# Optimization experiments

Hardware: AMD Instinct MI355X
Metric: run time of the kernel (lower is better)

The kernel has to match this reference:

```python
import jax, jax.numpy as jnp
import numpy as np

BN_EPS = 1e-5
NEG_SLOPE = 0.2

def _avgpool2(x):
    B, C, H, W = x.shape
    return x.reshape(B, C, H // 2, 2, W // 2, 2).mean(axis=(3, 5))

def _conv1x1(x, w, b):
    # x: [B,C,H,W], w: [O,C], b: [O]
    return jnp.einsum('bchw,oc->bohw', x, w) + b[None, :, None, None]

def _bilinear_resize(x, out_h, out_w):
    # PyTorch F.interpolate(mode='bilinear', align_corners=False) semantics
    B, C, h, w = x.shape
    ys = jnp.maximum((jnp.arange(out_h, dtype=jnp.float32) + 0.5) * (h / out_h) - 0.5, 0.0)
    xs = jnp.maximum((jnp.arange(out_w, dtype=jnp.float32) + 0.5) * (w / out_w) - 0.5, 0.0)
    y0 = jnp.floor(ys).astype(jnp.int32); x0 = jnp.floor(xs).astype(jnp.int32)
    wy = (ys - y0.astype(jnp.float32)).astype(x.dtype)
    wx = (xs - x0.astype(jnp.float32)).astype(x.dtype)
    y1 = jnp.minimum(y0 + 1, h - 1); x1 = jnp.minimum(x0 + 1, w - 1)
    rows = x[:, :, y0, :] * (1.0 - wy)[None, None, :, None] + x[:, :, y1, :] * wy[None, None, :, None]
    out = rows[:, :, :, x0] * (1.0 - wx)[None, None, None, :] + rows[:, :, :, x1] * wx[None, None, None, :]
    return out

def setup_inputs() -> dict:
    key = jax.random.key(0)
    ks = jax.random.split(key, 16)
    B, Cin, Hid, Cout, H, W = 8, 64, 64, 64, 128, 128
    s = 0.05
    return {
        'rgb': jax.random.normal(ks[0], (B, Cin, H, W), dtype=jnp.float32),
        'freq': jax.random.normal(ks[1], (B, Cin, H, W), dtype=jnp.float32),
        'w_q': jax.random.normal(ks[2], (Hid, Cin), dtype=jnp.float32) * s,
        'b_q': jax.random.normal(ks[3], (Hid,), dtype=jnp.float32) * s,
        'w_k': jax.random.normal(ks[4], (Hid, Cin), dtype=jnp.float32) * s,
        'b_k': jax.random.normal(ks[5], (Hid,), dtype=jnp.float32) * s,
        'w_v': jax.random.normal(ks[6], (Hid, Cin), dtype=jnp.float32) * s,
        'b_v': jax.random.normal(ks[7], (Hid,), dtype=jnp.float32) * s,
        'w_o': jax.random.normal(ks[8], (Cout, Hid), dtype=jnp.float32) * s,
        'b_o': jax.random.normal(ks[9], (Cout,), dtype=jnp.float32) * s,
        'bn_gamma': jnp.ones((Cout,), dtype=jnp.float32),
        'bn_beta': jnp.zeros((Cout,), dtype=jnp.float32),
        'bn_mean': jax.random.normal(ks[10], (Cout,), dtype=jnp.float32) * s,
        'bn_var': jax.random.uniform(ks[11], (Cout,), dtype=jnp.float32, minval=0.5, maxval=1.5),
    }

def reference(rgb, freq, w_q, b_q, w_k, b_k, w_v, b_v, w_o, b_o, bn_gamma, bn_beta, bn_mean, bn_var):
    B, C, H, W = rgb.shape
    rgb_ds = _avgpool2(rgb)
    freq_ds = _avgpool2(freq)
    hd, wd = rgb_ds.shape[2], rgb_ds.shape[3]
    hid = w_q.shape[0]
    scale = hid ** (-0.5)
    # 1x1 conv QKV projections, flatten spatial dims to tokens N = hd*wd
    q = _conv1x1(rgb_ds, w_q, b_q).reshape(B, hid, hd * wd)   # [B,hid,N]
    k = _conv1x1(freq_ds, w_k, b_k).reshape(B, hid, hd * wd)  # [B,hid,N]
    v = _conv1x1(freq_ds, w_v, b_v).reshape(B, hid, hd * wd)  # [B,hid,N]
    attn = jax.nn.softmax(jnp.einsum('bcn,bcm->bnm', q, k) * scale, axis=-1)  # [B,N,N]
    z = jnp.einsum('bnm,bcm->bcn', attn, v).reshape(B, hid, hd, wd)
    z = _bilinear_resize(z, H, W)
    y = _conv1x1(z, w_o, b_o)
    # inference-mode BatchNorm fused as affine
    inv = bn_gamma / jnp.sqrt(bn_var + BN_EPS)
    y = (y - bn_mean[None, :, None, None]) * inv[None, :, None, None] + bn_beta[None, :, None, None]
    y = jnp.where(y >= 0, y, NEG_SLOPE * y)  # LeakyReLU(0.2)
    return rgb + y
```

## Files before the change

### kernel.cpp

```cpp
#include <hip/hip_runtime.h>
#include <hip/hip_bf16.h>

typedef unsigned short u16;
typedef unsigned int   u32;
typedef __attribute__((ext_vector_type(8))) short bf16x8;
typedef __attribute__((ext_vector_type(4))) float f32x4;

__device__ __forceinline__ u16 f2bf(float f) {
  u32 u = __float_as_uint(f);
  u32 r = u + 0x7fffu + ((u >> 16) & 1u);
  return (u16)(r >> 16);
}
__device__ __forceinline__ float bflo(u32 u) { return __uint_as_float(u << 16); }
__device__ __forceinline__ float bfhi(u32 u) { return __uint_as_float(u & 0xffff0000u); }
__device__ __forceinline__ u32 packhi(float a, float b) {
  return __builtin_amdgcn_perm(__float_as_uint(b), __float_as_uint(a), 0x07060302u);
}

__global__ __launch_bounds__(256, 4) void k_qkv(
    const float* __restrict__ rgb, const float* __restrict__ freq,
    const float* __restrict__ wq, const float* __restrict__ bq,
    const float* __restrict__ wk, const float* __restrict__ bk,
    const float* __restrict__ wv, const float* __restrict__ bv,
    u16* __restrict__ Qo, u16* __restrict__ Ko, u16* __restrict__ Vo)
{
  __shared__ __align__(16) u16 sm[3 * 4608];
  u16* X  = sm;
  u16* W0 = sm + 4608;
  u16* W1 = sm + 9216;

  const int t    = threadIdx.x;
  const int side = blockIdx.x & 1;
  const int seg  = blockIdx.x >> 1;
  const int idx0 = seg * 64;
  const int bb   = idx0 >> 12;
  const int n0   = idx0 & 4095;
  const int h    = n0 >> 6;
  const float* src = side ? freq : rgb;

  const size_t sbase = (size_t)bb * 64 * 16384 + (size_t)(2 * h) * 128;
  for (int i = 0; i < 2; ++i) {
    int cell = i * 256 + t;
    int tok  = cell & 63;
    int grp  = cell >> 6;
    const float* p0 = src + sbase + 2 * tok + (size_t)(grp * 8) * 16384;
    u32 pk[4];
#pragma unroll
    for (int cc = 0; cc < 8; cc += 2) {
      const float* pa = p0 + (size_t)cc * 16384;
      float2 a0 = *(const float2*)pa;
      float2 a1 = *(const float2*)(pa + 128);
      float v0 = 0.25f * ((a0.x + a0.y) + (a1.x + a1.y));
      const float* pb = pa + 16384;
      float2 b0 = *(const float2*)pb;
      float2 b1 = *(const float2*)(pb + 128);
      float v1 = 0.25f * ((b0.x + b0.y) + (b1.x + b1.y));
      pk[cc >> 1] = (u32)f2bf(v0) | ((u32)f2bf(v1) << 16);
    }
    uint4 q4; q4.x = pk[0]; q4.y = pk[1]; q4.z = pk[2]; q4.w = pk[3];
    *(uint4*)&X[tok * 72 + grp * 8] = q4;
  }
  {
    const int o = t >> 2, c0 = (t & 3) << 4;
    const float4* p4 = (const float4*)((side ? wk : wq) + o * 64 + c0);
    float4 f0 = p4[0], f1 = p4[1], f2 = p4[2], f3 = p4[3];
    uint4 qa, qb;
    qa.x = (u32)f2bf(f0.x) | ((u32)f2bf(f0.y) << 16);
    qa.y = (u32)f2bf(f0.z) | ((u32)f2bf(f0.w) << 16);
    qa.z = (u32)f2bf(f1.x) | ((u32)f2bf(f1.y) << 16);
    qa.w = (u32)f2bf(f1.z) | ((u32)f2bf(f1.w) << 16);
    qb.x = (u32)f2bf(f2.x) | ((u32)f2bf(f2.y) << 16);
    qb.y = (u32)f2bf(f2.z) | ((u32)f2bf(f2.w) << 16);
    qb.z = (u32)f2bf(f3.x) | ((u32)f2bf(f3.y) << 16);
    qb.w = (u32)f2bf(f3.z) | ((u32)f2bf(f3.w) << 16);
    *(uint4*)&W0[o * 72 + c0] = qa;
    *(uint4*)&W0[o * 72 + c0 + 8] = qb;
    if (side) {
      const float4* v4 = (const float4*)(wv + o * 64 + c0);
      float4 g0 = v4[0], g1 = v4[1], g2 = v4[2], g3 = v4[3];
      qa.x = (u32)f2bf(g0.x) | ((u32)f2bf(g0.y) << 16);
      qa.y = (u32)f2bf(g0.z) | ((u32)f2bf(g0.w) << 16);
      qa.z = (u32)f2bf(g1.x) | ((u32)f2bf(g1.y) << 16);
      qa.w = (u32)f2bf(g1.z) | ((u32)f2bf(g1.w) << 16);
      qb.x = (u32)f2bf(g2.x) | ((u32)f2bf(g2.y) << 16);
      qb.y = (u32)f2bf(g2.z) | ((u32)f2bf(g2.w) << 16);
      qb.z = (u32)f2bf(g3.x) | ((u32)f2bf(g3.y) << 16);
      qb.w = (u32)f2bf(g3.z) | ((u32)f2bf(g3.w) << 16);
      *(uint4*)&W1[o * 72 + c0] = qa;
      *(uint4*)&W1[o * 72 + c0 + 8] = qb;
    }
  }
  __syncthreads();

  const int lane = t & 63, w = t >> 6;
  const int l15 = lane & 15, qd = lane >> 4;
  const int tb = w * 16;

  bf16x8 af0 = *(const bf16x8*)&X[(tb + l15) * 72 + qd * 8];
  bf16x8 af1 = *(const bf16x8*)&X[(tb + l15) * 72 + 32 + qd * 8];

  f32x4 acc[4];
#pragma unroll
  for (int nt = 0; nt < 4; ++nt) {
    bf16x8 b0 = *(const bf16x8*)&W0[(nt * 16 + l15) * 72 + qd * 8];
    bf16x8 b1 = *(const bf16x8*)&W0[(nt * 16 + l15) * 72 + 32 + qd * 8];
    f32x4 a = {0.f, 0.f, 0.f, 0.f};
    a = __builtin_amdgcn_mfma_f32_16x16x32_bf16(af0, b0, a, 0, 0, 0);
    a = __builtin_amdgcn_mfma_f32_16x16x32_bf16(af1, b1, a, 0, 0, 0);
    acc[nt] = a;
  }
  {
    const float* bias0 = side ? bk : bq;
    const float sc = side ? 1.f : 0.125f;
    u16* dst0 = side ? Ko : Qo;
#pragma unroll
    for (int nt = 0; nt < 4; ++nt) {
      float bia = bias0[nt * 16 + l15];
#pragma unroll
      for (int e = 0; e < 4; ++e) {
        int tok = idx0 + tb + qd * 4 + e;
        dst0[(size_t)tok * 64 + nt * 16 + l15] = f2bf((acc[nt][e] + bia) * sc);
      }
    }
  }

  if (side) {
    f32x4 accv[4];
#pragma unroll
    for (int ct = 0; ct < 4; ++ct) {
      bf16x8 a0 = *(const bf16x8*)&W1[(ct * 16 + l15) * 72 + qd * 8];
      bf16x8 a1 = *(const bf16x8*)&W1[(ct * 16 + l15) * 72 + 32 + qd * 8];
      f32x4 a = {0.f, 0.f, 0.f, 0.f};
      a = __builtin_amdgcn_mfma_f32_16x16x32_bf16(a0, af0, a, 0, 0, 0);
      a = __builtin_amdgcn_mfma_f32_16x16x32_bf16(a1, af1, a, 0, 0, 0);
      accv[ct] = a;
    }
#pragma unroll
    for (int ct = 0; ct < 4; ++ct) {
#pragma unroll
      for (int e = 0; e < 4; ++e) {
        int c = ct * 16 + qd * 4 + e;
        float v = accv[ct][e] + bv[c];
        Vo[((size_t)(bb * 64 + c)) * 4096 + n0 + tb + l15] = f2bf(v);
      }
    }
  }
}

__global__ __launch_bounds__(256, 2) void k_attn(
    const u16* __restrict__ Qg, const u16* __restrict__ Kg,
    const u16* __restrict__ Vg,
    const float* __restrict__ wo, const float* __restrict__ bo,
    const float* __restrict__ gam, const float* __restrict__ bet,
    const float* __restrict__ mean, const float* __restrict__ var,
    u16* __restrict__ Ya)
{
  __shared__ __align__(16) u16 Pb[4 * 4608];
  __shared__ __align__(16) u16 Wl[4608];
  __shared__ __align__(16) u16 Zc[4608];
  __shared__ float lb[256];

  const int b  = blockIdx.x;
  const int q0 = blockIdx.y * 64;
  const int t  = threadIdx.x;
  const int lane = t & 63, w = t >> 6;
  const int l15 = lane & 15, qd = lane >> 4;
  u16* P = Pb + w * 4608;

  {
    const int o = t >> 2, c0 = (t & 3) << 4;
    const float4* p4 = (const float4*)(wo + o * 64 + c0);
    float4 f0 = p4[0], f1 = p4[1], f2 = p4[2], f3 = p4[3];
    uint4 qa, qb;
    qa.x = (u32)f2bf(f0.x) | ((u32)f2bf(f0.y) << 16);
    qa.y = (u32)f2bf(f0.z) | ((u32)f2bf(f0.w) << 16);
    qa.z = (u32)f2bf(f1.x) | ((u32)f2bf(f1.y) << 16);
    qa.w = (u32)f2bf(f1.z) | ((u32)f2bf(f1.w) << 16);
    qb.x = (u32)f2bf(f2.x) | ((u32)f2bf(f2.y) << 16);
    qb.y = (u32)f2bf(f2.z) | ((u32)f2bf(f2.w) << 16);
    qb.z = (u32)f2bf(f3.x) | ((u32)f2bf(f3.y) << 16);
    qb.w = (u32)f2bf(f3.z) | ((u32)f2bf(f3.w) << 16);
    *(uint4*)&Wl[o * 72 + c0] = qa;
    *(uint4*)&Wl[o * 72 + c0 + 8] = qb;
  }

  bf16x8 qf[4][2];
#pragma unroll
  for (int qt = 0; qt < 4; ++qt) {
    const u16* p = Qg + ((size_t)(b * 4096 + q0 + qt * 16 + l15)) * 64 + qd * 8;
    qf[qt][0] = *(const bf16x8*)p;
    qf[qt][1] = *(const bf16x8*)(p + 32);
  }

  f32x4 zacc[4][4];
#pragma unroll
  for (int i = 0; i < 4; ++i)
#pragma unroll
    for (int j = 0; j < 4; ++j) {
      f32x4 z = {0.f, 0.f, 0.f, 0.f};
      zacc[i][j] = z;
    }
  float lacc[4] = {0.f, 0.f, 0.f, 0.f};

  for (int tile = 0; tile < 16; ++tile) {
    const int n0 = w * 1024 + tile * 64;

    bf16x8 kf[4][2], vf[4][2];
#pragma unroll
    for (int mt = 0; mt < 4; ++mt) {
      const u16* p = Kg + ((size_t)(b * 4096 + n0 + mt * 16 + l15)) * 64 + qd * 8;
      kf[mt][0] = *(const bf16x8*)p;
      kf[mt][1] = *(const bf16x8*)(p + 32);
    }
#pragma unroll
    for (int ct = 0; ct < 4; ++ct) {
      const u16* p = Vg + ((size_t)(b * 64 + ct * 16 + l15)) * 4096 + n0 + qd * 8;
      vf[ct][0] = *(const bf16x8*)p;
      vf[ct][1] = *(const bf16x8*)(p + 32);
    }

#pragma unroll
    for (int qt = 0; qt < 4; ++qt) {
#pragma unroll
      for (int mt = 0; mt < 4; ++mt) {
        f32x4 a = {0.f, 0.f, 0.f, 0.f};
        a = __builtin_amdgcn_mfma_f32_16x16x32_bf16(kf[mt][0], qf[qt][0], a, 0, 0, 0);
        a = __builtin_amdgcn_mfma_f32_16x16x32_bf16(kf[mt][1], qf[qt][1], a, 0, 0, 0);
        float p0 = __expf(a[0]);
        float p1 = __expf(a[1]);
        float p2 = __expf(a[2]);
        float p3 = __expf(a[3]);
        lacc[qt] += (p0 + p1) + (p2 + p3);
        uint2 pw;
        pw.x = packhi(p0, p1);
        pw.y = packhi(p2, p3);
        *(uint2*)&P[(qt * 16 + l15) * 72 + mt * 16 + qd * 4] = pw;
      }
    }
#pragma unroll
    for (int qt = 0; qt < 4; ++qt) {
      bf16x8 pf0 = *(const bf16x8*)&P[(qt * 16 + l15) * 72 + qd * 8];
      bf16x8 pf1 = *(const bf16x8*)&P[(qt * 16 + l15) * 72 + 32 + qd * 8];
#pragma unroll
      for (int ct = 0; ct < 4; ++ct) {
        zacc[ct][qt] = __builtin_amdgcn_mfma_f32_16x16x32_bf16(vf[ct][0], pf0, zacc[ct][qt], 0, 0, 0);
        zacc[ct][qt] = __builtin_amdgcn_mfma_f32_16x16x32_bf16(vf[ct][1], pf1, zacc[ct][qt], 0, 0, 0);
      }
    }
  }

#pragma unroll
  for (int qt = 0; qt < 4; ++qt) {
    float l = lacc[qt];
    l += __shfl_xor(l, 16);
    l += __shfl_xor(l, 32);
    lb[w * 64 + qt * 16 + l15] = l;
  }
#pragma unroll
  for (int qt = 0; qt < 4; ++qt)
#pragma unroll
    for (int ct = 0; ct < 4; ++ct) {
      uint2 pw;
      pw.x = packhi(zacc[ct][qt][0], zacc[ct][qt][1]);
      pw.y = packhi(zacc[ct][qt][2], zacc[ct][qt][3]);
      *(uint2*)&P[(qt * 16 + l15) * 72 + ct * 16 + qd * 4] = pw;
    }
  __syncthreads();

  {
    const u32* Pu = (const u32*)Pb;
    u32* Zu = (u32*)Zc;
#pragma unroll
    for (int i = 0; i < 8; ++i) {
      int cell = i * 256 + t;
      int q = cell >> 5, cu = cell & 31;
      float s0 = 0.f, s1 = 0.f;
#pragma unroll
      for (int ww = 0; ww < 4; ++ww) {
        u32 v = Pu[ww * 2304 + q * 36 + cu];
        s0 += bflo(v);
        s1 += bfhi(v);
      }
      float inv = 1.f / (lb[q] + lb[64 + q] + lb[128 + q] + lb[192 + q]);
      Zu[q * 36 + cu] = packhi(s0 * inv, s1 * inv);
    }
  }
  __syncthreads();

  {
    bf16x8 af0 = *(const bf16x8*)&Zc[(w * 16 + l15) * 72 + qd * 8];
    bf16x8 af1 = *(const bf16x8*)&Zc[(w * 16 + l15) * 72 + 32 + qd * 8];
#pragma unroll
    for (int nt = 0; nt < 4; ++nt) {
      bf16x8 b0 = *(const bf16x8*)&Wl[(nt * 16 + l15) * 72 + qd * 8];
      bf16x8 b1 = *(const bf16x8*)&Wl[(nt * 16 + l15) * 72 + 32 + qd * 8];
      f32x4 y = {0.f, 0.f, 0.f, 0.f};
      y = __builtin_amdgcn_mfma_f32_16x16x32_bf16(af0, b0, y, 0, 0, 0);
      y = __builtin_amdgcn_mfma_f32_16x16x32_bf16(af1, b1, y, 0, 0, 0);
      const int o = nt * 16 + l15;
      float A = gam[o] * __frsqrt_rn(var[o] + 1e-5f);
      float B = (bo[o] - mean[o]) * A + bet[o];
#pragma unroll
      for (int e = 0; e < 4; ++e) {
        float v = y[e] * A + B;
        size_t tok = (size_t)(b * 4096 + q0 + w * 16 + qd * 4 + e);
        Ya[tok * 64 + o] = (u16)(__float_as_uint(v) >> 16);
      }
    }
  }
}

__global__ __launch_bounds__(256, 4) void k_out(
    const u16* __restrict__ Ya, const float* __restrict__ rgb,
    float* __restrict__ out)
{
  const int px = blockIdx.x * 256 + threadIdx.x;
  const int j = px & 127;
  const int i = (px >> 7) & 127;
  const int b = px >> 14;

  float ys = fmaxf((i + 0.5f) * 0.5f - 0.5f, 0.f);
  int   y0 = (int)ys;
  float wy = ys - (float)y0;
  int   y1 = min(y0 + 1, 63);
  float xs = fmaxf((j + 0.5f) * 0.5f - 0.5f, 0.f);
  int   x0 = (int)xs;
  float wx = xs - (float)x0;
  int   x1 = min(x0 + 1, 63);
  float w00 = (1.f - wy) * (1.f - wx), w01 = (1.f - wy) * wx;
  float w10 = wy * (1.f - wx),         w11 = wy * wx;

  const u16* yb = Ya + (size_t)b * 262144;
  const int b00 = (y0 * 64 + x0) * 64, b01 = (y0 * 64 + x1) * 64;
  const int b10 = (y1 * 64 + x0) * 64, b11 = (y1 * 64 + x1) * 64;

#pragma unroll
  for (int ch = 0; ch < 8; ++ch) {
    uint4 a00 = *(const uint4*)&yb[b00 + ch * 8];
    uint4 a01 = *(const uint4*)&yb[b01 + ch * 8];
    uint4 a10 = *(const uint4*)&yb[b10 + ch * 8];
    uint4 a11 = *(const uint4*)&yb[b11 + ch * 8];
    const u32* u00 = (const u32*)&a00;
    const u32* u01 = (const u32*)&a01;
    const u32* u10 = (const u32*)&a10;
    const u32* u11 = (const u32*)&a11;
#pragma unroll
    for (int e = 0; e < 8; ++e) {
      const int wd = e >> 1;
      float c00 = (e & 1) ? bfhi(u00[wd]) : bflo(u00[wd]);
      float c01 = (e & 1) ? bfhi(u01[wd]) : bflo(u01[wd]);
      float c10 = (e & 1) ? bfhi(u10[wd]) : bflo(u10[wd]);
      float c11 = (e & 1) ? bfhi(u11[wd]) : bflo(u11[wd]);
      float v = w00 * c00 + w01 * c01 + w10 * c10 + w11 * c11;
      v = (v >= 0.f) ? v : 0.2f * v;
      const int o = ch * 8 + e;
      const size_t oi = ((size_t)((b * 64 + o) * 128 + i)) * 128 + j;
      out[oi] = rgb[oi] + v;
    }
  }
}

extern "C" void kernel_launch(void* const* d_in, const int* in_sizes, int n_in,
                              void* d_out, int out_size, void* d_ws, size_t ws_size,
                              hipStream_t stream) {
  (void)in_sizes; (void)n_in; (void)out_size; (void)ws_size;
  const float* rgb  = (const float*)d_in[0];
  const float* freq = (const float*)d_in[1];
  const float* wq   = (const float*)d_in[2];
  const float* bq   = (const float*)d_in[3];
  const float* wk   = (const float*)d_in[4];
  const float* bk   = (const float*)d_in[5];
  const float* wv   = (const float*)d_in[6];
  const float* bv   = (const float*)d_in[7];
  const float* wo   = (const float*)d_in[8];
  const float* bo   = (const float*)d_in[9];
  const float* gam  = (const float*)d_in[10];
  const float* bet  = (const float*)d_in[11];
  const float* mean = (const float*)d_in[12];
  const float* var  = (const float*)d_in[13];

  char* ws = (char*)d_ws;
  u16* Qw = (u16*)(ws);
  u16* Kw = (u16*)(ws + 4194304);
  u16* Vw = (u16*)(ws + 8388608);
  u16* Yw = (u16*)(ws + 12582912);

  k_qkv<<<dim3(1024), dim3(256), 0, stream>>>(rgb, freq, wq, bq, wk, bk, wv, bv,
                                              Qw, Kw, Vw);
  k_attn<<<dim3(8, 64), dim3(256), 0, stream>>>(Qw, Kw, Vw, wo, bo, gam, bet,
                                                mean, var, Yw);
  k_out<<<dim3(512), dim3(256), 0, stream>>>(Yw, rgb, (float*)d_out);
}
```

Before: 229.3 us.

## Double-buffer K/V register loads and use exp2 with log2e-prescaled Q

After: 253.9 us. 10.7% more time.

```diff
diff --git a/kernel.cpp b/kernel.cpp
--- a/kernel.cpp
+++ b/kernel.cpp
@@ -111,7 +111,7 @@
   }
   {
     const float* bias0 = side ? bk : bq;
-    const float sc = side ? 1.f : 0.125f;
+    const float sc = side ? 1.f : 0.18033688f;
     u16* dst0 = side ? Ko : Qo;
 #pragma unroll
     for (int nt = 0; nt < 4; ++nt) {
@@ -202,52 +202,65 @@
     }
   float lacc[4] = {0.f, 0.f, 0.f, 0.f};
 
-  for (int tile = 0; tile < 16; ++tile) {
-    const int n0 = w * 1024 + tile * 64;
-
-    bf16x8 kf[4][2], vf[4][2];
-#pragma unroll
-    for (int mt = 0; mt < 4; ++mt) {
-      const u16* p = Kg + ((size_t)(b * 4096 + n0 + mt * 16 + l15)) * 64 + qd * 8;
-      kf[mt][0] = *(const bf16x8*)p;
-      kf[mt][1] = *(const bf16x8*)(p + 32);
-    }
-#pragma unroll
-    for (int ct = 0; ct < 4; ++ct) {
-      const u16* p = Vg + ((size_t)(b * 64 + ct * 16 + l15)) * 4096 + n0 + qd * 8;
-      vf[ct][0] = *(const bf16x8*)p;
-      vf[ct][1] = *(const bf16x8*)(p + 32);
-    }
-
-#pragma unroll
-    for (int qt = 0; qt < 4; ++qt) {
-#pragma unroll
-      for (int mt = 0; mt < 4; ++mt) {
-        f32x4 a = {0.f, 0.f, 0.f, 0.f};
-        a = __builtin_amdgcn_mfma_f32_16x16x32_bf16(kf[mt][0], qf[qt][0], a, 0, 0, 0);
-        a = __builtin_amdgcn_mfma_f32_16x16x32_bf16(kf[mt][1], qf[qt][1], a, 0, 0, 0);
-        float p0 = __expf(a[0]);
-        float p1 = __expf(a[1]);
-        float p2 = __expf(a[2]);
-        float p3 = __expf(a[3]);
-        lacc[qt] += (p0 + p1) + (p2 + p3);
-        uint2 pw;
-        pw.x = packhi(p0, p1);
-        pw.y = packhi(p2, p3);
-        *(uint2*)&P[(qt * 16 + l15) * 72 + mt * 16 + qd * 4] = pw;
-      }
-    }
-#pragma unroll
-    for (int qt = 0; qt < 4; ++qt) {
-      bf16x8 pf0 = *(const bf16x8*)&P[(qt * 16 + l15) * 72 + qd * 8];
-      bf16x8 pf1 = *(const bf16x8*)&P[(qt * 16 + l15) * 72 + 32 + qd * 8];
-#pragma unroll
-      for (int ct = 0; ct < 4; ++ct) {
-        zacc[ct][qt] = __builtin_amdgcn_mfma_f32_16x16x32_bf16(vf[ct][0], pf0, zacc[ct][qt], 0, 0, 0);
-        zacc[ct][qt] = __builtin_amdgcn_mfma_f32_16x16x32_bf16(vf[ct][1], pf1, zacc[ct][qt], 0, 0, 0);
-      }
-    }
-  }
+#define LOAD_KV(KF, VF, TILE)                                                 \
+  do {                                                                        \
+    const int nn = w * 1024 + (TILE) * 64;                                    \
+    _Pragma("unroll")                                                         \
+    for (int mt = 0; mt < 4; ++mt) {                                          \
+      const u16* p = Kg + ((size_t)(b * 4096 + nn + mt * 16 + l15)) * 64 + qd * 8; \
+      KF[mt][0] = *(const bf16x8*)p;                                          \
+      KF[mt][1] = *(const bf16x8*)(p + 32);                                   \
+    }                                                                         \
+    _Pragma("unroll")                                                         \
+    for (int ct = 0; ct < 4; ++ct) {                                          \
+      const u16* p = Vg + ((size_t)(b * 64 + ct * 16 + l15)) * 4096 + nn + qd * 8; \
+      VF[ct][0] = *(const bf16x8*)p;                                          \
+      VF[ct][1] = *(const bf16x8*)(p + 32);                                   \
+    }                                                                         \
+  } while (0)
+
+#define TILE_COMPUTE(KF, VF)                                                  \
+  do {                                                                        \
+    _Pragma("unroll")                                                         \
+    for (int qt = 0; qt < 4; ++qt) {                                          \
+      _Pragma("unroll")                                                       \
+      for (int mt = 0; mt < 4; ++mt) {                                        \
+        f32x4 a = {0.f, 0.f, 0.f, 0.f};                                       \
+        a = __builtin_amdgcn_mfma_f32_16x16x32_bf16(KF[mt][0], qf[qt][0], a, 0, 0, 0); \
+        a = __builtin_amdgcn_mfma_f32_16x16x32_bf16(KF[mt][1], qf[qt][1], a, 0, 0, 0); \
+        float p0 = __builtin_amdgcn_exp2f(a[0]);                              \
+        float p1 = __builtin_amdgcn_exp2f(a[1]);                              \
+        float p2 = __builtin_amdgcn_exp2f(a[2]);                              \
+        float p3 = __builtin_amdgcn_exp2f(a[3]);                              \
+        lacc[qt] += (p0 + p1) + (p2 + p3);                                    \
+        uint2 pw;                                                             \
+        pw.x = packhi(p0, p1);                                                \
+        pw.y = packhi(p2, p3);                                                \
+        *(uint2*)&P[(qt * 16 + l15) * 72 + mt * 16 + qd * 4] = pw;            \
+      }                                                                       \
+    }                                                                         \
+    _Pragma("unroll")                                                         \
+    for (int qt = 0; qt < 4; ++qt) {                                          \
+      bf16x8 pf0 = *(const bf16x8*)&P[(qt * 16 + l15) * 72 + qd * 8];         \
+      bf16x8 pf1 = *(const bf16x8*)&P[(qt * 16 + l15) * 72 + 32 + qd * 8];    \
+      _Pragma("unroll")                                                       \
+      for (int ct = 0; ct < 4; ++ct) {                                        \
+        zacc[ct][qt] = __builtin_amdgcn_mfma_f32_16x16x32_bf16(VF[ct][0], pf0, zacc[ct][qt], 0, 0, 0); \
+        zacc[ct][qt] = __builtin_amdgcn_mfma_f32_16x16x32_bf16(VF[ct][1], pf1, zacc[ct][qt], 0, 0, 0); \
+      }                                                                       \
+    }                                                                         \
+  } while (0)
+
+  bf16x8 kfA[4][2], vfA[4][2], kfB[4][2], vfB[4][2];
+  LOAD_KV(kfA, vfA, 0);
+  for (int it = 0; it < 8; ++it) {
+    LOAD_KV(kfB, vfB, 2 * it + 1);
+    TILE_COMPUTE(kfA, vfA);
+    if (it < 7) LOAD_KV(kfA, vfA, 2 * it + 2);
+    TILE_COMPUTE(kfB, vfB);
+  }
+#undef LOAD_KV
+#undef TILE_COMPUTE
 
 #pragma unroll
   for (int qt = 0; qt < 4; ++qt) {
```

## Split attention block into 8 waves over query halves and use exp2

Applied to the files above, without the earlier changes.

After: 287.6 us. 1.25x slower.

```diff
diff --git a/kernel.cpp b/kernel.cpp
--- a/kernel.cpp
+++ b/kernel.cpp
@@ -111,7 +111,7 @@
   }
   {
     const float* bias0 = side ? bk : bq;
-    const float sc = side ? 1.f : 0.125f;
+    const float sc = side ? 1.f : 0.18033688f;
     u16* dst0 = side ? Ko : Qo;
 #pragma unroll
     for (int nt = 0; nt < 4; ++nt) {
@@ -147,7 +147,7 @@
   }
 }
 
-__global__ __launch_bounds__(256, 2) void k_attn(
+__global__ __launch_bounds__(512, 4) void k_attn(
     const u16* __restrict__ Qg, const u16* __restrict__ Kg,
     const u16* __restrict__ Vg,
     const float* __restrict__ wo, const float* __restrict__ bo,
@@ -155,7 +155,7 @@
     const float* __restrict__ mean, const float* __restrict__ var,
     u16* __restrict__ Ya)
 {
-  __shared__ __align__(16) u16 Pb[4 * 4608];
+  __shared__ __align__(16) u16 Pb[8 * 2304];
   __shared__ __align__(16) u16 Wl[4608];
   __shared__ __align__(16) u16 Zc[4608];
   __shared__ float lb[256];
@@ -164,72 +164,62 @@
   const int q0 = blockIdx.y * 64;
   const int t  = threadIdx.x;
   const int lane = t & 63, w = t >> 6;
+  const int qh = w >> 2, ks = w & 3;
   const int l15 = lane & 15, qd = lane >> 4;
-  u16* P = Pb + w * 4608;
-
-  {
-    const int o = t >> 2, c0 = (t & 3) << 4;
+  u16* P = Pb + w * 2304;
+
+  {
+    const int o = t >> 3, c0 = (t & 7) << 3;
     const float4* p4 = (const float4*)(wo + o * 64 + c0);
-    float4 f0 = p4[0], f1 = p4[1], f2 = p4[2], f3 = p4[3];
-    uint4 qa, qb;
+    float4 f0 = p4[0], f1 = p4[1];
+    uint4 qa;
     qa.x = (u32)f2bf(f0.x) | ((u32)f2bf(f0.y) << 16);
     qa.y = (u32)f2bf(f0.z) | ((u32)f2bf(f0.w) << 16);
     qa.z = (u32)f2bf(f1.x) | ((u32)f2bf(f1.y) << 16);
     qa.w = (u32)f2bf(f1.z) | ((u32)f2bf(f1.w) << 16);
-    qb.x = (u32)f2bf(f2.x) | ((u32)f2bf(f2.y) << 16);
-    qb.y = (u32)f2bf(f2.z) | ((u32)f2bf(f2.w) << 16);
-    qb.z = (u32)f2bf(f3.x) | ((u32)f2bf(f3.y) << 16);
-    qb.w = (u32)f2bf(f3.z) | ((u32)f2bf(f3.w) << 16);
     *(uint4*)&Wl[o * 72 + c0] = qa;
-    *(uint4*)&Wl[o * 72 + c0 + 8] = qb;
-  }
-
-  bf16x8 qf[4][2];
-#pragma unroll
-  for (int qt = 0; qt < 4; ++qt) {
-    const u16* p = Qg + ((size_t)(b * 4096 + q0 + qt * 16 + l15)) * 64 + qd * 8;
+  }
+
+  bf16x8 qf[2][2];
+#pragma unroll
+  for (int qt = 0; qt < 2; ++qt) {
+    const u16* p = Qg + ((size_t)(b * 4096 + q0 + qh * 32 + qt * 16 + l15)) * 64 + qd * 8;
     qf[qt][0] = *(const bf16x8*)p;
     qf[qt][1] = *(const bf16x8*)(p + 32);
   }
 
-  f32x4 zacc[4][4];
+  f32x4 zacc[4][2];
 #pragma unroll
   for (int i = 0; i < 4; ++i)
 #pragma unroll
-    for (int j = 0; j < 4; ++j) {
+    for (int j = 0; j < 2; ++j) {
       f32x4 z = {0.f, 0.f, 0.f, 0.f};
       zacc[i][j] = z;
     }
-  float lacc[4] = {0.f, 0.f, 0.f, 0.f};
+  float lacc[2] = {0.f, 0.f};
 
   for (int tile = 0; tile < 16; ++tile) {
-    const int n0 = w * 1024 + tile * 64;
-
-    bf16x8 kf[4][2], vf[4][2];
+    const int nn = ks * 1024 + tile * 64;
+
+    bf16x8 kf[4][2];
 #pragma unroll
     for (int mt = 0; mt < 4; ++mt) {
-      const u16* p = Kg + ((size_t)(b * 4096 + n0 + mt * 16 + l15)) * 64 + qd * 8;
+      const u16* p = Kg + ((size_t)(b * 4096 + nn + mt * 16 + l15)) * 64 + qd * 8;
       kf[mt][0] = *(const bf16x8*)p;
       kf[mt][1] = *(const bf16x8*)(p + 32);
     }
-#pragma unroll
-    for (int ct = 0; ct < 4; ++ct) {
-      const u16* p = Vg + ((size_t)(b * 64 + ct * 16 + l15)) * 4096 + n0 + qd * 8;
-      vf[ct][0] = *(const bf16x8*)p;
-      vf[ct][1] = *(const bf16x8*)(p + 32);
-    }
-
-#pragma unroll
-    for (int qt = 0; qt < 4; ++qt) {
+
+#pragma unroll
+    for (int qt = 0; qt < 2; ++qt) {
 #pragma unroll
       for (int mt = 0; mt < 4; ++mt) {
         f32x4 a = {0.f, 0.f, 0.f, 0.f};
         a = __builtin_amdgcn_mfma_f32_16x16x32_bf16(kf[mt][0], qf[qt][0], a, 0, 0, 0);
         a = __builtin_amdgcn_mfma_f32_16x16x32_bf16(kf[mt][1], qf[qt][1], a, 0, 0, 0);
-        float p0 = __expf(a[0]);
-        float p1 = __expf(a[1]);
-        float p2 = __expf(a[2]);
-        float p3 = __expf(a[3]);
+        float p0 = __builtin_amdgcn_exp2f(a[0]);
+        float p1 = __builtin_amdgcn_exp2f(a[1]);
+        float p2 = __builtin_amdgcn_exp2f(a[2]);
+        float p3 = __builtin_amdgcn_exp2f(a[3]);
         lacc[qt] += (p0 + p1) + (p2 + p3);
         uint2 pw;
         pw.x = packhi(p0, p1);
@@ -237,8 +227,17 @@
         *(uint2*)&P[(qt * 16 + l15) * 72 + mt * 16 + qd * 4] = pw;
       }
     }
-#pragma unroll
-    for (int qt = 0; qt < 4; ++qt) {
+
+    bf16x8 vf[4][2];
+#pragma unroll
+    for (int ct = 0; ct < 4; ++ct) {
+      const u16* p = Vg + ((size_t)(b * 64 + ct * 16 + l15)) * 4096 + nn + qd * 8;
+      vf[ct][0] = *(const bf16x8*)p;
+      vf[ct][1] = *(const bf16x8*)(p + 32);
+    }
+
+#pragma unroll
+    for (int qt = 0; qt < 2; ++qt) {
       bf16x8 pf0 = *(const bf16x8*)&P[(qt * 16 + l15) * 72 + qd * 8];
       bf16x8 pf1 = *(const bf16x8*)&P[(qt * 16 + l15) * 72 + 32 + qd * 8];
 #pragma unroll
@@ -250,14 +249,14 @@
   }
 
 #pragma unroll
-  for (int qt = 0; qt < 4; ++qt) {
+  for (int qt = 0; qt < 2; ++qt) {
     float l = lacc[qt];
     l += __shfl_xor(l, 16);
     l += __shfl_xor(l, 32);
-    lb[w * 64 + qt * 16 + l15] = l;
-  }
-#pragma unroll
-  for (int qt = 0; qt < 4; ++qt)
+    lb[w * 32 + qt * 16 + l15] = l;
+  }
+#pragma unroll
+  for (int qt = 0; qt < 2; ++qt)
 #pragma unroll
     for (int ct = 0; ct < 4; ++ct) {
       uint2 pw;
@@ -271,27 +270,32 @@
     const u32* Pu = (const u32*)Pb;
     u32* Zu = (u32*)Zc;
 #pragma unroll
-    for (int i = 0; i < 8; ++i) {
-      int cell = i * 256 + t;
+    for (int i = 0; i < 4; ++i) {
+      int cell = i * 512 + t;
       int q = cell >> 5, cu = cell & 31;
+      int qh2 = q >> 5, qq = q & 31;
       float s0 = 0.f, s1 = 0.f;
+      float den = 0.f;
 #pragma unroll
       for (int ww = 0; ww < 4; ++ww) {
-        u32 v = Pu[ww * 2304 + q * 36 + cu];
+        u32 v = Pu[(qh2 * 4 + ww) * 1152 + qq * 36 + cu];
         s0 += bflo(v);
         s1 += bfhi(v);
-      }
-      float inv = 1.f / (lb[q] + lb[64 + q] + lb[128 + q] + lb[192 + q]);
+        den += lb[(qh2 * 4 + ww) * 32 + qq];
+      }
+      float inv = 1.f / den;
       Zu[q * 36 + cu] = packhi(s0 * inv, s1 * inv);
     }
   }
   __syncthreads();
 
   {
-    bf16x8 af0 = *(const bf16x8*)&Zc[(w * 16 + l15) * 72 + qd * 8];
-    bf16x8 af1 = *(const bf16x8*)&Zc[(w * 16 + l15) * 72 + 32 + qd * 8];
-#pragma unroll
-    for (int nt = 0; nt < 4; ++nt) {
+    const int qr = w & 3, oh = w >> 2;
+    bf16x8 af0 = *(const bf16x8*)&Zc[(qr * 16 + l15) * 72 + qd * 8];
+    bf16x8 af1 = *(const bf16x8*)&Zc[(qr * 16 + l15) * 72 + 32 + qd * 8];
+#pragma unroll
+    for (int ni = 0; ni < 2; ++ni) {
+      const int nt = oh * 2 + ni;
       bf16x8 b0 = *(const bf16x8*)&Wl[(nt * 16 + l15) * 72 + qd * 8];
       bf16x8 b1 = *(const bf16x8*)&Wl[(nt * 16 + l15) * 72 + 32 + qd * 8];
       f32x4 y = {0.f, 0.f, 0.f, 0.f};
@@ -303,7 +307,7 @@
 #pragma unroll
       for (int e = 0; e < 4; ++e) {
         float v = y[e] * A + B;
-        size_t tok = (size_t)(b * 4096 + q0 + w * 16 + qd * 4 + e);
+        size_t tok = (size_t)(b * 4096 + q0 + qr * 16 + qd * 4 + e);
         Ya[tok * 64 + o] = (u16)(__float_as_uint(v) >> 16);
       }
     }
@@ -387,7 +391,7 @@
 
   k_qkv<<<dim3(1024), dim3(256), 0, stream>>>(rgb, freq, wq, bq, wk, bk, wv, bv,
                                               Qw, Kw, Vw);
-  k_attn<<<dim3(8, 64), dim3(256), 0, stream>>>(Qw, Kw, Vw, wo, bo, gam, bet,
+  k_attn<<<dim3(8, 64), dim3(512), 0, stream>>>(Qw, Kw, Vw, wo, bo, gam, bet,
                                                 mean, var, Yw);
   k_out<<<dim3(512), dim3(256), 0, stream>>>(Yw, rgb, (float*)d_out);
 }
```
